# Performance work log

Hardware: AMD Instinct MI355X
Metric: run time of the kernel (lower is better)

Reference implementation:

```python
import jax, jax.numpy as jnp
import numpy as np

LAMBDA_D = 250.0
POS_MARGIN = 1.0
NEG_MARGIN = 0.2
BLOCK = 8          # block_size in the original
DIST_THRESH = 7.5  # correspondence threshold in pixels
EPS = 1e-12        # F.normalize eps


def _l2_normalize(x, axis):
    # matches torch.nn.functional.normalize: x / max(||x||_2, eps)
    n = jnp.linalg.norm(x, axis=axis, keepdims=True)
    return x / jnp.maximum(n, EPS)


def setup_inputs() -> dict:
    key = jax.random.key(0)
    k1, k2, k3 = jax.random.split(key, 3)
    b, d, hc, wc = 2, 256, 60, 80  # 480x640 image, block 8
    desc = jax.random.normal(k1, (b, d, hc, wc), dtype=jnp.float32)
    wrap_desc = jax.random.normal(k2, (b, d, hc, wc), dtype=jnp.float32)
    # realistic near-identity homographies (random H would warp everything off-image)
    H = jnp.eye(3, dtype=jnp.float32)[None] + 0.02 * jax.random.normal(k3, (b, 3, 3), dtype=jnp.float32)
    return {"desc": desc, "wrap_desc": wrap_desc, "H": H}


def reference(desc, wrap_desc, H):
    b, d, hc, wc = desc.shape
    n = hc * wc

    # cell-center coordinates in (row, col) order, shape (hc, wc, 2)
    coords = jnp.stack(
        jnp.meshgrid(jnp.arange(hc), jnp.arange(wc), indexing="ij"), axis=-1
    ).astype(jnp.float32) * BLOCK + BLOCK // 2

    # homogeneous (x, y, 1) points, shape (n, 3)
    xy1 = jnp.concatenate(
        [coords[..., 1:2], coords[..., 0:1], jnp.ones((hc, wc, 1), jnp.float32)],
        axis=-1,
    ).reshape(n, 3)

    # warp by homography: (b, n, 3)
    w = jnp.einsum("bij,nj->bni", H, xy1)
    wxy = w[..., :2] / w[..., 2:3]                       # (b, n, 2) in (x, y)
    warp = jnp.stack([wxy[..., 1], wxy[..., 0]], axis=-1).reshape(b, hc, wc, 2)  # (row, col)

    # distance between warped query centers and all cell centers: (b, hc, wc, hc, wc)
    dist = jnp.linalg.norm(coords[None, None, None] - warp[:, :, :, None, None, :], axis=-1)
    S = (dist <= DIST_THRESH).astype(desc.dtype)

    # unit-normalized descriptors, channel-last
    dn = _l2_normalize(jnp.transpose(desc, (0, 2, 3, 1)), axis=-1)       # (b, hc, wc, d)
    wn = _l2_normalize(jnp.transpose(wrap_desc, (0, 2, 3, 1)), axis=-1)  # (b, hc, wc, d)

    # full correlation volume via batched GEMM (same math as broadcast-sum)
    dot = jax.nn.relu(jnp.einsum("bijd,bkld->bijkl", dn, wn))           # (b,hc,wc,hc,wc)

    # normalize over warped-cell axis (k, l), then over query-cell axis (i, j)
    dot = _l2_normalize(dot.reshape(b, hc, wc, n), axis=3).reshape(b, hc, wc, hc, wc)
    dot = _l2_normalize(dot.reshape(b, n, hc, wc), axis=1).reshape(b, hc, wc, hc, wc)

    loss = LAMBDA_D * S * jax.nn.relu(POS_MARGIN - dot) + (1.0 - S) * jax.nn.relu(dot - NEG_MARGIN)
    # sum over (i,j,k,l) per image / n^2, then sum over batch == total sum / n^2
    return jnp.sum(loss) / float(n * n)
```

## Files before the change

kernel.cpp:

```cpp
#include <hip/hip_runtime.h>

#define HC 60
#define WCC 80
#define NCELL 4800
#define NP 4864
#define NB 38
#define DCH 256
#define BATCH 2
#define QT 64

typedef _Float16 half8 __attribute__((ext_vector_type(8)));
typedef float f32x4 __attribute__((ext_vector_type(4)));

__device__ __forceinline__ void gload_lds16(const void* gp, void* lp) {
  __builtin_amdgcn_global_load_lds(
      (const __attribute__((address_space(1))) void*)gp,
      (__attribute__((address_space(3))) void*)lp, 16, 0, 0);
}

__global__ __launch_bounds__(256) void warp_kernel(const float* __restrict__ H,
                                                   float* __restrict__ wout) {
  int idx = blockIdx.x * 256 + threadIdx.x;
  if (idx >= BATCH * NP) return;
  int b = idx / NP;
  int q = idx - b * NP;
  float wr = 1e9f, wc = 1e9f;
  if (q < NCELL) {
    int i = q / WCC;
    int j = q - i * WCC;
    float x = (float)(j * 8 + 4);
    float y = (float)(i * 8 + 4);
    const float* h = H + b * 9;
    float w0 = h[0] * x + h[1] * y + h[2];
    float w1 = h[3] * x + h[4] * y + h[5];
    float w2 = h[6] * x + h[7] * y + h[8];
    wr = w1 / w2;
    wc = w0 / w2;
  }
  wout[2 * idx]     = wr;
  wout[2 * idx + 1] = wc;
}

__global__ __launch_bounds__(256) void normalize_kernel(
    const float* __restrict__ desc, const float* __restrict__ wdesc,
    _Float16* __restrict__ dnp, _Float16* __restrict__ wnp) {
  __shared__ _Float16 vt[DCH][QT + 2];
  __shared__ float pss[4][QT];
  __shared__ float invq[QT];
  const int q0 = blockIdx.x * QT;
  const int which = blockIdx.y;
  const int b = blockIdx.z;
  const float* in = which ? wdesc : desc;
  _Float16* out = which ? wnp : dnp;
  const int tx = threadIdx.x & 63;
  const int ty = threadIdx.x >> 6;
  const int q = q0 + tx;
  float ss = 0.f;
  for (int cc = 0; cc < DCH / 4; ++cc) {
    const int c = cc * 4 + ty;
    float v = (q < NCELL) ? in[((size_t)b * DCH + c) * NCELL + q] : 0.f;
    vt[c][tx] = (_Float16)v;
    ss += v * v;
  }
  pss[ty][tx] = ss;
  __syncthreads();
  if (ty == 0) {
    float tot = pss[0][tx] + pss[1][tx] + pss[2][tx] + pss[3][tx];
    invq[tx] = 1.f / fmaxf(sqrtf(tot), 1e-12f);
  }
  __syncthreads();
  for (int it = 0; it < QT; ++it) {
    out[((size_t)b * NP + q0 + it) * DCH + threadIdx.x] =
        (_Float16)((float)vt[threadIdx.x][it] * invq[it]);
  }
}

template <int MODE>
__global__ __launch_bounds__(256, 2) void gemm_kernel(
    const _Float16* __restrict__ A, const _Float16* __restrict__ Bm,
    const float* __restrict__ rowsq, const float* __restrict__ colsq,
    const float* __restrict__ warp, float* __restrict__ sqacc,
    float* __restrict__ lossp) {
  __shared__ _Float16 As[128][128];
  __shared__ _Float16 Bs[128][128];
  const int tid = threadIdx.x;
  const int wave = tid >> 6;
  const int lane = tid & 63;
  const int batch = blockIdx.z;
  const int row0 = blockIdx.y * 128;
  const int col0 = blockIdx.x * 128;
  const _Float16* Ab = A + ((size_t)batch * NP + row0) * DCH;
  const _Float16* Bb = Bm + ((size_t)batch * NP + col0) * DCH;

  const int wq_r = wave >> 1;
  const int wq_c = wave & 1;
  const int g = lane >> 4;
  const int cL = lane & 15;

  f32x4 acc[4][4] = {};

  const int srow4 = lane >> 4;
  const int sunit = lane & 15;

  for (int ks = 0; ks < 2; ++ks) {
#pragma unroll
    for (int c = 0; c < 8; ++c) {
      const int chunk = wave * 8 + c;
      const int r = chunk * 4 + srow4;
      const int gcol = ks * 128 + ((sunit ^ (r & 15)) << 3);
      gload_lds16(Ab + (size_t)r * DCH + gcol,
                  (char*)(&As[0][0]) + chunk * 1024);
      gload_lds16(Bb + (size_t)r * DCH + gcol,
                  (char*)(&Bs[0][0]) + chunk * 1024);
    }
    __syncthreads();
#pragma unroll
    for (int kk = 0; kk < 4; ++kk) {
      half8 af[4], bf[4];
#pragma unroll
      for (int m = 0; m < 4; ++m) {
        const int row = wq_r * 64 + m * 16 + cL;
        const int u16 = (kk * 4 + g) ^ (row & 15);
        af[m] = *reinterpret_cast<const half8*>(
            (const char*)(&As[0][0]) + row * 256 + u16 * 16);
      }
#pragma unroll
      for (int n = 0; n < 4; ++n) {
        const int row = wq_c * 64 + n * 16 + cL;
        const int u16 = (kk * 4 + g) ^ (row & 15);
        bf[n] = *reinterpret_cast<const half8*>(
            (const char*)(&Bs[0][0]) + row * 256 + u16 * 16);
      }
#pragma unroll
      for (int m = 0; m < 4; ++m)
#pragma unroll
        for (int n = 0; n < 4; ++n)
          acc[m][n] =
              __builtin_amdgcn_mfma_f32_16x16x32_f16(af[m], bf[n], acc[m][n], 0, 0, 0);
    }
    __syncthreads();
  }

  if (MODE == 0 || MODE == 1) {
    float cs[4];
    if (MODE == 1) {
#pragma unroll
      for (int n = 0; n < 4; ++n) {
        float v = colsq[(size_t)batch * NP + col0 + wq_c * 64 + n * 16 + cL];
        cs[n] = 1.f / fmaxf(sqrtf(v), 1e-12f);
      }
    }
    float rs[4][4];
#pragma unroll
    for (int m = 0; m < 4; ++m)
#pragma unroll
      for (int j = 0; j < 4; ++j) rs[m][j] = 0.f;
#pragma unroll
    for (int m = 0; m < 4; ++m)
#pragma unroll
      for (int n = 0; n < 4; ++n)
#pragma unroll
        for (int j = 0; j < 4; ++j) {
          float u = fmaxf(acc[m][n][j], 0.f);
          if (MODE == 1) u *= cs[n];
          rs[m][j] += u * u;
        }
#pragma unroll
    for (int m = 0; m < 4; ++m)
#pragma unroll
      for (int j = 0; j < 4; ++j) {
        float v = rs[m][j];
        v += __shfl_xor(v, 1, 64);
        v += __shfl_xor(v, 2, 64);
        v += __shfl_xor(v, 4, 64);
        v += __shfl_xor(v, 8, 64);
        if (cL == 0)
          atomicAdd(&sqacc[(size_t)batch * NP + row0 + wq_r * 64 + m * 16 + g * 4 + j], v);
      }
  } else {
    float cy[4], cx[4], ic[4];
    int cvalid[4];
#pragma unroll
    for (int n = 0; n < 4; ++n) {
      int ct = col0 + wq_c * 64 + n * 16 + cL;
      cvalid[n] = (ct < NCELL);
      int tk = ct / WCC;
      int tl = ct - tk * WCC;
      cy[n] = (float)(tk * 8 + 4);
      cx[n] = (float)(tl * 8 + 4);
      ic[n] = 1.f / fmaxf(sqrtf(colsq[(size_t)batch * NP + ct]), 1e-12f);
    }
    float lsum = 0.f;
#pragma unroll
    for (int m = 0; m < 4; ++m)
#pragma unroll
      for (int j = 0; j < 4; ++j) {
        const int rq = row0 + wq_r * 64 + m * 16 + g * 4 + j;
        if (rq < NCELL) {
          const float ir =
              1.f / fmaxf(sqrtf(rowsq[(size_t)batch * NP + rq]), 1e-12f);
          const float wrr = warp[((size_t)batch * NP + rq) * 2];
          const float wcol = warp[((size_t)batch * NP + rq) * 2 + 1];
#pragma unroll
          for (int n = 0; n < 4; ++n) {
            if (cvalid[n]) {
              float u = fmaxf(acc[m][n][j], 0.f);
              float v = u * ir * ic[n];
              float dr = cy[n] - wrr;
              float dc = cx[n] - wcol;
              float pos = 250.f * fmaxf(1.f - v, 0.f);
              float neg = fmaxf(v - 0.2f, 0.f);
              lsum += (dr * dr + dc * dc <= 56.25f) ? pos : neg;
            }
          }
        }
      }
#pragma unroll
    for (int s = 1; s < 64; s <<= 1) lsum += __shfl_xor(lsum, s, 64);
    if (lane == 0) {
      int slot = (((batch * NB + blockIdx.y) * NB + blockIdx.x) << 2) | wave;
      lossp[slot] = lsum;
    }
  }
}

__global__ __launch_bounds__(1024) void loss_reduce(const float* __restrict__ lossp,
                                                    float* __restrict__ out, int count) {
  double s = 0.0;
  for (int i = threadIdx.x; i < count; i += 1024) s += (double)lossp[i];
#pragma unroll
  for (int k = 1; k < 64; k <<= 1) s += __shfl_xor(s, k, 64);
  __shared__ double sd[16];
  if ((threadIdx.x & 63) == 0) sd[threadIdx.x >> 6] = s;
  __syncthreads();
  if (threadIdx.x == 0) {
    double t = 0.0;
    for (int w = 0; w < 16; ++w) t += sd[w];
    out[0] = (float)(t / ((double)NCELL * (double)NCELL));
  }
}

extern "C" void kernel_launch(void* const* d_in, const int* in_sizes, int n_in,
                              void* d_out, int out_size, void* d_ws, size_t ws_size,
                              hipStream_t stream) {
  const float* desc  = (const float*)d_in[0];
  const float* wdesc = (const float*)d_in[1];
  const float* H     = (const float*)d_in[2];
  char* ws = (char*)d_ws;

  constexpr size_t SZ_HALF = (size_t)BATCH * NP * DCH * sizeof(_Float16);
  constexpr size_t SZ_WARP = (size_t)BATCH * NP * 2 * sizeof(float);
  constexpr size_t SZ_VEC  = (size_t)BATCH * NP * sizeof(float);
  constexpr size_t OFF_DNP  = 0;
  constexpr size_t OFF_WNP  = OFF_DNP + SZ_HALF;
  constexpr size_t OFF_WARP = OFF_WNP + SZ_HALF;
  constexpr size_t OFF_R2   = OFF_WARP + SZ_WARP;
  constexpr size_t OFF_C2   = OFF_R2 + SZ_VEC;
  constexpr size_t OFF_LOSS = OFF_C2 + SZ_VEC;

  _Float16* dnp = (_Float16*)(ws + OFF_DNP);
  _Float16* wnp = (_Float16*)(ws + OFF_WNP);
  float* warp = (float*)(ws + OFF_WARP);
  float* r2   = (float*)(ws + OFF_R2);
  float* c2   = (float*)(ws + OFF_C2);
  float* lossp = (float*)(ws + OFF_LOSS);

  hipMemsetAsync(r2, 0, 2 * SZ_VEC, stream);

  warp_kernel<<<dim3((BATCH * NP + 255) / 256), 256, 0, stream>>>(H, warp);
  normalize_kernel<<<dim3(NP / QT, 2, BATCH), 256, 0, stream>>>(desc, wdesc, dnp, wnp);

  dim3 gg(NB, NB, BATCH);
  gemm_kernel<0><<<gg, 256, 0, stream>>>(dnp, wnp, nullptr, nullptr, nullptr, r2, nullptr);
  gemm_kernel<1><<<gg, 256, 0, stream>>>(wnp, dnp, nullptr, r2, nullptr, c2, nullptr);
  gemm_kernel<2><<<gg, 256, 0, stream>>>(dnp, wnp, r2, c2, warp, nullptr, lossp);
  loss_reduce<<<1, 1024, 0, stream>>>(lossp, (float*)d_out, BATCH * NB * NB * 4);
}
```

Before: 300.0 us.

## Issue all K-slice loads upfront and wait per slice with vmcnt

The GEMM now splits the 256-wide K dimension into four 64-wide LDS slices and issues every global-to-LDS load for all slices before any compute. Each slice waits on a partial vmcnt count plus a barrier, so MFMA work on early slices overlaps with loads still in flight, and the trailing syncthreads are gone. The swizzle is adapted to 128-byte rows. The occupancy hint of two blocks per CU is dropped, which frees the compiler's register budget but may lower occupancy.

```diff
diff --git a/kernel.cpp b/kernel.cpp
--- a/kernel.cpp
+++ b/kernel.cpp
@@ -76,13 +76,13 @@
 }
 
 template <int MODE>
-__global__ __launch_bounds__(256, 2) void gemm_kernel(
+__global__ __launch_bounds__(256) void gemm_kernel(
     const _Float16* __restrict__ A, const _Float16* __restrict__ Bm,
     const float* __restrict__ rowsq, const float* __restrict__ colsq,
     const float* __restrict__ warp, float* __restrict__ sqacc,
     float* __restrict__ lossp) {
-  __shared__ _Float16 As[128][128];
-  __shared__ _Float16 Bs[128][128];
+  __shared__ _Float16 As[4][128][64];
+  __shared__ _Float16 Bs[4][128][64];
   const int tid = threadIdx.x;
   const int wave = tid >> 6;
   const int lane = tid & 63;
@@ -99,37 +99,47 @@
 
   f32x4 acc[4][4] = {};
 
-  const int srow4 = lane >> 4;
-  const int sunit = lane & 15;
-
-  for (int ks = 0; ks < 2; ++ks) {
-#pragma unroll
-    for (int c = 0; c < 8; ++c) {
-      const int chunk = wave * 8 + c;
-      const int r = chunk * 4 + srow4;
-      const int gcol = ks * 128 + ((sunit ^ (r & 15)) << 3);
-      gload_lds16(Ab + (size_t)r * DCH + gcol,
-                  (char*)(&As[0][0]) + chunk * 1024);
-      gload_lds16(Bb + (size_t)r * DCH + gcol,
-                  (char*)(&Bs[0][0]) + chunk * 1024);
-    }
-    __syncthreads();
-#pragma unroll
-    for (int kk = 0; kk < 4; ++kk) {
+  const int srow = lane >> 3;
+  const int scol = lane & 7;
+  const int sc_swz = (scol ^ srow) * 8;
+
+#pragma unroll
+  for (int ks = 0; ks < 4; ++ks) {
+#pragma unroll
+    for (int c = 0; c < 4; ++c) {
+      const int chunk = wave * 4 + c;
+      const int r = chunk * 8 + srow;
+      gload_lds16(Ab + (size_t)r * DCH + ks * 64 + sc_swz,
+                  (char*)(&As[ks][0][0]) + chunk * 1024);
+      gload_lds16(Bb + (size_t)r * DCH + ks * 64 + sc_swz,
+                  (char*)(&Bs[ks][0][0]) + chunk * 1024);
+    }
+  }
+
+#pragma unroll
+  for (int ks = 0; ks < 4; ++ks) {
+    if (ks == 0)      asm volatile("s_waitcnt vmcnt(24)" ::: "memory");
+    else if (ks == 1) asm volatile("s_waitcnt vmcnt(16)" ::: "memory");
+    else if (ks == 2) asm volatile("s_waitcnt vmcnt(8)" ::: "memory");
+    else              asm volatile("s_waitcnt vmcnt(0)" ::: "memory");
+    __builtin_amdgcn_s_barrier();
+    asm volatile("" ::: "memory");
+#pragma unroll
+    for (int kk = 0; kk < 2; ++kk) {
       half8 af[4], bf[4];
 #pragma unroll
       for (int m = 0; m < 4; ++m) {
         const int row = wq_r * 64 + m * 16 + cL;
-        const int u16 = (kk * 4 + g) ^ (row & 15);
+        const int c16 = (kk * 4 + g) ^ (row & 7);
         af[m] = *reinterpret_cast<const half8*>(
-            (const char*)(&As[0][0]) + row * 256 + u16 * 16);
+            (const char*)(&As[ks][0][0]) + row * 128 + c16 * 16);
       }
 #pragma unroll
       for (int n = 0; n < 4; ++n) {
         const int row = wq_c * 64 + n * 16 + cL;
-        const int u16 = (kk * 4 + g) ^ (row & 15);
+        const int c16 = (kk * 4 + g) ^ (row & 7);
         bf[n] = *reinterpret_cast<const half8*>(
-            (const char*)(&Bs[0][0]) + row * 256 + u16 * 16);
+            (const char*)(&Bs[ks][0][0]) + row * 128 + c16 * 16);
       }
 #pragma unroll
       for (int m = 0; m < 4; ++m)
@@ -138,7 +148,6 @@
           acc[m][n] =
               __builtin_amdgcn_mfma_f32_16x16x32_f16(af[m], bf[n], acc[m][n], 0, 0, 0);
     }
-    __syncthreads();
   }
 
   if (MODE == 0 || MODE == 1) {
@@ -199,14 +208,14 @@
         if (rq < NCELL) {
           const float ir =
               1.f / fmaxf(sqrtf(rowsq[(size_t)batch * NP + rq]), 1e-12f);
-          const float wrr = warp[((size_t)batch * NP + rq) * 2];
+          const float wr = warp[((size_t)batch * NP + rq) * 2];
           const float wcol = warp[((size_t)batch * NP + rq) * 2 + 1];
 #pragma unroll
           for (int n = 0; n < 4; ++n) {
             if (cvalid[n]) {
               float u = fmaxf(acc[m][n][j], 0.f);
               float v = u * ir * ic[n];
-              float dr = cy[n] - wrr;
+              float dr = cy[n] - wr;
               float dc = cx[n] - wcol;
               float pos = 250.f * fmaxf(1.f - v, 0.f);
               float neg = fmaxf(v - 0.2f, 0.f);
```

Result: slower. 412.3 us (+37.4%).
